# Optimization experiments

Measured on AMD Instinct MI355X. Metric: run time of the kernel, lower is better.

Reference implementation:

```python
import jax, jax.numpy as jnp
import numpy as np

H = 64      # LSTM hidden units
OUT = 10    # dense softmax classes


def setup_inputs() -> dict:
    key = jax.random.key(0)
    k0, k1, k2, k3 = jax.random.split(key, 4)
    B, T, D = 256, 1024, 128
    x = jax.random.normal(k0, (B, T, D), dtype=jnp.float32)
    # small weight scale keeps relu cell state stable over 1024 steps
    W = jax.random.normal(k1, (D, 4 * H), dtype=jnp.float32) * 0.05
    U = jax.random.normal(k2, (H, 4 * H), dtype=jnp.float32) * 0.05
    b = jnp.zeros((4 * H,), jnp.float32)
    Wd = jax.random.normal(k3, (H, OUT), dtype=jnp.float32) * 0.05
    bd = jnp.zeros((OUT,), jnp.float32)
    return {"x": x, "W": W, "U": U, "b": b, "Wd": Wd, "bd": bd}


def hard_sigmoid(z):
    # legacy Keras recurrent_activation default
    return jnp.clip(0.2 * z + 0.5, 0.0, 1.0)


def lstm_last_hidden(x, W, U, b):
    # x: [B,T,D] -> last hidden state [B,H]
    B = x.shape[0]
    xw = jnp.einsum('btd,dg->btg', x, W) + b  # [B,T,4H] input projection, computed once

    def step(carry, xt):
        h, c = carry
        z = xt + h @ U  # [B,4H]
        i = hard_sigmoid(z[:, :H])
        f = hard_sigmoid(z[:, H:2 * H])
        g = jax.nn.relu(z[:, 2 * H:3 * H])   # activation='relu' (candidate)
        o = hard_sigmoid(z[:, 3 * H:])
        c = f * c + i * g
        h = o * jax.nn.relu(c)               # activation='relu' on cell output
        return (h, c), None

    h0 = jnp.zeros((B, H), x.dtype)
    (h, _), _ = jax.lax.scan(step, (h0, h0), jnp.swapaxes(xw, 0, 1))
    return h


def reference(x, W, U, b, Wd, bd):
    h = lstm_last_hidden(x, W, U, b)          # [B,H]
    return jax.nn.softmax(h @ Wd + bd, axis=-1)  # [B,OUT]
```

## Files before the change

### kernel.cpp

```cpp
#include <hip/hip_runtime.h>
#include <hip/hip_bf16.h>

#define Hh   64
#define G4   256
#define Dd   128
#define Bsz  256
#define Tt   1024
#define NOUT 10

typedef __bf16  bf16x8 __attribute__((ext_vector_type(8)));
typedef float   f32x4v __attribute__((ext_vector_type(4)));

__global__ __launch_bounds__(128)
void k0_wt(const float* __restrict__ W, __bf16* __restrict__ Wt) {
    const int n = blockIdx.x;
    const int k = threadIdx.x;
    Wt[(size_t)n * Dd + k] = (__bf16)W[(size_t)k * G4 + n];
}

#define K1_RT 8

__global__ __launch_bounds__(256)
void k1_mfma(const float* __restrict__ x, const __bf16* __restrict__ Wt,
             const float* __restrict__ bias, __bf16* __restrict__ xw) {
    const int tid = threadIdx.x;
    const int w   = tid >> 6;
    const int l   = tid & 63;
    const int r16 = l & 15;
    const int kq  = l >> 4;
    const size_t rowbase = (size_t)blockIdx.x * (16 * K1_RT);

    bf16x8 bfr[4][4];
    float  bval[4];
#pragma unroll
    for (int ct = 0; ct < 4; ++ct) {
        const int col = w * 64 + ct * 16 + r16;
        const __bf16* wp = Wt + (size_t)col * Dd + kq * 8;
#pragma unroll
        for (int kk = 0; kk < 4; ++kk)
            bfr[ct][kk] = *(const bf16x8*)(wp + kk * 32);
        bval[ct] = bias[col];
    }

    for (int rt = 0; rt < K1_RT; ++rt) {
        const size_t arow = rowbase + rt * 16 + r16;
        const float* xr = x + arow * Dd + kq * 8;
        bf16x8 afr[4];
#pragma unroll
        for (int kk = 0; kk < 4; ++kk) {
            const float4 lo = *(const float4*)(xr + kk * 32);
            const float4 hi = *(const float4*)(xr + kk * 32 + 4);
            afr[kk][0] = (__bf16)lo.x; afr[kk][1] = (__bf16)lo.y;
            afr[kk][2] = (__bf16)lo.z; afr[kk][3] = (__bf16)lo.w;
            afr[kk][4] = (__bf16)hi.x; afr[kk][5] = (__bf16)hi.y;
            afr[kk][6] = (__bf16)hi.z; afr[kk][7] = (__bf16)hi.w;
        }
        f32x4v acc[4];
#pragma unroll
        for (int ct = 0; ct < 4; ++ct)
            acc[ct] = (f32x4v){bval[ct], bval[ct], bval[ct], bval[ct]};
#pragma unroll
        for (int ct = 0; ct < 4; ++ct)
#pragma unroll
            for (int kk = 0; kk < 4; ++kk)
                acc[ct] = __builtin_amdgcn_mfma_f32_16x16x32_bf16(
                              afr[kk], bfr[ct][kk], acc[ct], 0, 0, 0);

        const size_t orow0 = rowbase + rt * 16 + kq * 4;
#pragma unroll
        for (int ct = 0; ct < 4; ++ct) {
            const int col = w * 64 + ct * 16 + r16;
#pragma unroll
            for (int r = 0; r < 4; ++r)
                xw[(orow0 + r) * G4 + col] = (__bf16)acc[ct][r];
        }
    }
}

__global__ __launch_bounds__(256)
void k2_scan(const __bf16* __restrict__ xw, const float* __restrict__ U,
             float* __restrict__ hout) {
    const int g = threadIdx.x;
    const int brow = blockIdx.x;

    __shared__ __align__(16) float hs[Hh];
    __shared__ float zs[G4];

    float u[Hh];
#pragma unroll
    for (int j = 0; j < Hh; ++j) u[j] = U[(size_t)j * G4 + g];

    float c = 0.f;
    if (g < Hh) hs[g] = 0.f;

    const __bf16* __restrict__ xwcol = xw + (size_t)brow * Tt * G4 + g;
    float zin = (float)xwcol[0];
    __syncthreads();

    for (int t = 0; t < Tt; ++t) {
        const int tn = (t + 1 < Tt) ? (t + 1) : (Tt - 1);
        const float znext = (float)xwcol[(size_t)tn * G4];
        float a0 = zin, a1 = 0.f, a2 = 0.f, a3 = 0.f;
#pragma unroll
        for (int j = 0; j < Hh; j += 4) {
            const f32x4v h4 = *(const f32x4v*)&hs[j];
            a0 = fmaf(h4[0], u[j + 0], a0);
            a1 = fmaf(h4[1], u[j + 1], a1);
            a2 = fmaf(h4[2], u[j + 2], a2);
            a3 = fmaf(h4[3], u[j + 3], a3);
        }
        zs[g] = (a0 + a1) + (a2 + a3);
        __syncthreads();
        if (g < Hh) {
            const float zi = zs[g], zf = zs[Hh + g], zg = zs[2 * Hh + g], zo = zs[3 * Hh + g];
            const float gi = fminf(fmaxf(0.2f * zi + 0.5f, 0.f), 1.f);
            const float gf = fminf(fmaxf(0.2f * zf + 0.5f, 0.f), 1.f);
            const float gg = fmaxf(zg, 0.f);
            const float go = fminf(fmaxf(0.2f * zo + 0.5f, 0.f), 1.f);
            c = gf * c + gi * gg;
            hs[g] = go * fmaxf(c, 0.f);
        }
        zin = znext;
        __syncthreads();
    }
    if (g < Hh) hout[(size_t)brow * Hh + g] = hs[g];
}

__global__ __launch_bounds__(256)
void k3_dense(const float* __restrict__ hin, const float* __restrict__ Wd,
              const float* __restrict__ bd, float* __restrict__ out) {
    __shared__ float wd[Hh * NOUT];
    __shared__ float bds[NOUT];
    for (int i = threadIdx.x; i < Hh * NOUT; i += blockDim.x) wd[i] = Wd[i];
    if (threadIdx.x < NOUT) bds[threadIdx.x] = bd[threadIdx.x];
    __syncthreads();

    const int r = threadIdx.x;
    if (r < Bsz) {
        float hrow[Hh];
#pragma unroll
        for (int j = 0; j < Hh; ++j) hrow[j] = hin[(size_t)r * Hh + j];
        float logits[NOUT];
#pragma unroll
        for (int o = 0; o < NOUT; ++o) {
            float acc = bds[o];
#pragma unroll
            for (int j = 0; j < Hh; ++j) acc = fmaf(hrow[j], wd[j * NOUT + o], acc);
            logits[o] = acc;
        }
        float m = logits[0];
#pragma unroll
        for (int o = 1; o < NOUT; ++o) m = fmaxf(m, logits[o]);
        float s = 0.f;
#pragma unroll
        for (int o = 0; o < NOUT; ++o) { logits[o] = expf(logits[o] - m); s += logits[o]; }
        const float inv = 1.f / s;
#pragma unroll
        for (int o = 0; o < NOUT; ++o) out[(size_t)r * NOUT + o] = logits[o] * inv;
    }
}

extern "C" void kernel_launch(void* const* d_in, const int* in_sizes, int n_in,
                              void* d_out, int out_size, void* d_ws, size_t ws_size,
                              hipStream_t stream) {
    const float* x  = (const float*)d_in[0];
    const float* W  = (const float*)d_in[1];
    const float* U  = (const float*)d_in[2];
    const float* b  = (const float*)d_in[3];
    const float* Wd = (const float*)d_in[4];
    const float* bd = (const float*)d_in[5];
    float* out = (float*)d_out;

    const size_t xw_bytes = (size_t)Bsz * Tt * G4 * sizeof(__bf16);
    __bf16* xw   = (__bf16*)d_ws;
    float*  hbuf = (float*)((char*)d_ws + xw_bytes);
    __bf16* Wt   = (__bf16*)((char*)d_ws + xw_bytes + (size_t)Bsz * Hh * sizeof(float));

    k0_wt<<<G4, Dd, 0, stream>>>(W, Wt);
    k1_mfma<<<(Bsz * Tt) / (16 * K1_RT), 256, 0, stream>>>(x, Wt, b, xw);
    k2_scan<<<Bsz, 256, 0, stream>>>(xw, U, hbuf);
    k3_dense<<<1, 256, 0, stream>>>(hbuf, Wd, bd, out);
}
```

Before: 572.0 us.

## Permute gate columns so LSTM scan gathers gates via wave shuffles

The projection kernel now writes gate columns in a permuted order, so each wavefront's lanes hold the i, f, g, o pre-activations for the same 16 hidden units. The scan kernel gathers the four gates with cross-lane shuffles and updates the cell state in every lane, instead of going through a shared zs buffer. With a double-buffered h array this removes one of the two block barriers per timestep. All lanes now compute the redundant cell update and a few extra shuffles run per step, traded against less barrier and LDS traffic in the serial 1024-step loop.

```diff
diff --git a/kernel.cpp b/kernel.cpp
--- a/kernel.cpp
+++ b/kernel.cpp
@@ -10,6 +10,7 @@
 
 typedef __bf16  bf16x8 __attribute__((ext_vector_type(8)));
 typedef float   f32x4v __attribute__((ext_vector_type(4)));
+
 
 __global__ __launch_bounds__(128)
 void k0_wt(const float* __restrict__ W, __bf16* __restrict__ Wt) {
@@ -69,10 +70,10 @@
         const size_t orow0 = rowbase + rt * 16 + kq * 4;
 #pragma unroll
         for (int ct = 0; ct < 4; ++ct) {
-            const int col = w * 64 + ct * 16 + r16;
+            const int pcol = ct * 64 + w * 16 + r16;
 #pragma unroll
             for (int r = 0; r < 4; ++r)
-                xw[(orow0 + r) * G4 + col] = (__bf16)acc[ct][r];
+                xw[(orow0 + r) * G4 + pcol] = (__bf16)acc[ct][r];
         }
     }
 }
@@ -80,50 +81,64 @@
 __global__ __launch_bounds__(256)
 void k2_scan(const __bf16* __restrict__ xw, const float* __restrict__ U,
              float* __restrict__ hout) {
-    const int g = threadIdx.x;
+    const int tid = threadIdx.x;
+    const int w   = tid >> 6;
+    const int l   = tid & 63;
+    const int q   = l >> 4;
+    const int m   = l & 15;
     const int brow = blockIdx.x;
 
-    __shared__ __align__(16) float hs[Hh];
-    __shared__ float zs[G4];
+    __shared__ __align__(16) float hs[2][Hh];
 
+    const int ucol = 64 * q + 16 * w + m;
     float u[Hh];
 #pragma unroll
-    for (int j = 0; j < Hh; ++j) u[j] = U[(size_t)j * G4 + g];
+    for (int j = 0; j < Hh; ++j) u[j] = U[(size_t)j * G4 + ucol];
 
     float c = 0.f;
-    if (g < Hh) hs[g] = 0.f;
+    if (tid < Hh) { hs[0][tid] = 0.f; }
 
-    const __bf16* __restrict__ xwcol = xw + (size_t)brow * Tt * G4 + g;
-    float zin = (float)xwcol[0];
+    const __bf16* __restrict__ xwrow = xw + (size_t)brow * Tt * G4 + tid;
+    float zin = (float)xwrow[0];
     __syncthreads();
 
     for (int t = 0; t < Tt; ++t) {
+        const int p  = t & 1;
         const int tn = (t + 1 < Tt) ? (t + 1) : (Tt - 1);
-        const float znext = (float)xwcol[(size_t)tn * G4];
+        const float znext = (float)xwrow[(size_t)tn * G4];
+
         float a0 = zin, a1 = 0.f, a2 = 0.f, a3 = 0.f;
 #pragma unroll
         for (int j = 0; j < Hh; j += 4) {
-            const f32x4v h4 = *(const f32x4v*)&hs[j];
+            const f32x4v h4 = *(const f32x4v*)&hs[p][j];
             a0 = fmaf(h4[0], u[j + 0], a0);
             a1 = fmaf(h4[1], u[j + 1], a1);
             a2 = fmaf(h4[2], u[j + 2], a2);
             a3 = fmaf(h4[3], u[j + 3], a3);
         }
-        zs[g] = (a0 + a1) + (a2 + a3);
-        __syncthreads();
-        if (g < Hh) {
-            const float zi = zs[g], zf = zs[Hh + g], zg = zs[2 * Hh + g], zo = zs[3 * Hh + g];
-            const float gi = fminf(fmaxf(0.2f * zi + 0.5f, 0.f), 1.f);
-            const float gf = fminf(fmaxf(0.2f * zf + 0.5f, 0.f), 1.f);
-            const float gg = fmaxf(zg, 0.f);
-            const float go = fminf(fmaxf(0.2f * zo + 0.5f, 0.f), 1.f);
-            c = gf * c + gi * gg;
-            hs[g] = go * fmaxf(c, 0.f);
-        }
+        const float z = (a0 + a1) + (a2 + a3);
+
+        const float v0 = z;
+        const float v1 = __shfl_xor(z, 16);
+        const float v2 = __shfl_xor(z, 32);
+        const float v3 = __shfl_xor(v1, 32);
+        const float zi = (q == 0) ? v0 : (q == 1) ? v1 : (q == 2) ? v2 : v3;
+        const float zf = (q == 1) ? v0 : (q == 0) ? v1 : (q == 3) ? v2 : v3;
+        const float zg = (q == 2) ? v0 : (q == 3) ? v1 : (q == 0) ? v2 : v3;
+        const float zo = (q == 3) ? v0 : (q == 2) ? v1 : (q == 1) ? v2 : v3;
+
+        const float gi = fminf(fmaxf(0.2f * zi + 0.5f, 0.f), 1.f);
+        const float gf = fminf(fmaxf(0.2f * zf + 0.5f, 0.f), 1.f);
+        const float gg = fmaxf(zg, 0.f);
+        const float go = fminf(fmaxf(0.2f * zo + 0.5f, 0.f), 1.f);
+        c = gf * c + gi * gg;
+        const float h = go * fmaxf(c, 0.f);
+
+        if (q == 0) hs[1 - p][16 * w + m] = h;
         zin = znext;
         __syncthreads();
     }
-    if (g < Hh) hout[(size_t)brow * Hh + g] = hs[g];
+    if (tid < Hh) hout[(size_t)brow * Hh + tid] = hs[0][tid];
 }
 
 __global__ __launch_bounds__(256)
@@ -148,12 +163,12 @@
             for (int j = 0; j < Hh; ++j) acc = fmaf(hrow[j], wd[j * NOUT + o], acc);
             logits[o] = acc;
         }
-        float m = logits[0];
+        float mx = logits[0];
 #pragma unroll
-        for (int o = 1; o < NOUT; ++o) m = fmaxf(m, logits[o]);
+        for (int o = 1; o < NOUT; ++o) mx = fmaxf(mx, logits[o]);
         float s = 0.f;
 #pragma unroll
-        for (int o = 0; o < NOUT; ++o) { logits[o] = expf(logits[o] - m); s += logits[o]; }
+        for (int o = 0; o < NOUT; ++o) { logits[o] = expf(logits[o] - mx); s += logits[o]; }
         const float inv = 1.f / s;
 #pragma unroll
         for (int o = 0; o < NOUT; ++o) out[(size_t)r * NOUT + o] = logits[o] * inv;
```

Result: slower. 619.0 us (+8.2%).

## Cut scan to one barrier per step using redundant gate math and double buffers

Applied to the files above, without the earlier changes.

The recurrent scan kernel now double-buffers the gate pre-activations and the hidden state, so each timestep needs one block barrier instead of two. Every wave computes the gate nonlinearities and cell update for all 64 units and keeps its own private copy of h, which removes the cross-wave dependency on h. Each block now handles two batch rows with 512 threads, and the xw prefetch looks two steps ahead. The cost is redundant elementwise work in every wave and only 128 blocks, which may leave half the CUs idle on a latency-bound loop.

```diff
diff --git a/kernel.cpp b/kernel.cpp
--- a/kernel.cpp
+++ b/kernel.cpp
@@ -71,59 +71,72 @@
         for (int ct = 0; ct < 4; ++ct) {
             const int col = w * 64 + ct * 16 + r16;
 #pragma unroll
-            for (int r = 0; r < 4; ++r)
-                xw[(orow0 + r) * G4 + col] = (__bf16)acc[ct][r];
+            for (int rr = 0; rr < 4; ++rr)
+                xw[(orow0 + rr) * G4 + col] = (__bf16)acc[ct][rr];
         }
     }
 }
 
-__global__ __launch_bounds__(256)
+#define RPB 2
+
+__global__ __launch_bounds__(512)
 void k2_scan(const __bf16* __restrict__ xw, const float* __restrict__ U,
              float* __restrict__ hout) {
-    const int g = threadIdx.x;
-    const int brow = blockIdx.x;
+    const int tid = threadIdx.x;
+    const int r   = tid >> 8;
+    const int g   = tid & 255;
+    const int w4  = g >> 6;
+    const int l   = g & 63;
+    const int brow = blockIdx.x * RPB + r;
 
-    __shared__ __align__(16) float hs[Hh];
-    __shared__ float zs[G4];
+    __shared__ float zs[2][RPB][G4];
+    __shared__ __align__(16) float hs[2][RPB][4][Hh];
 
     float u[Hh];
 #pragma unroll
     for (int j = 0; j < Hh; ++j) u[j] = U[(size_t)j * G4 + g];
 
     float c = 0.f;
-    if (g < Hh) hs[g] = 0.f;
+    hs[0][r][w4][l] = 0.f;
 
-    const __bf16* __restrict__ xwcol = xw + (size_t)brow * Tt * G4 + g;
-    float zin = (float)xwcol[0];
+    const __bf16* __restrict__ xwp = xw + (size_t)brow * Tt * G4 + g;
+    float zcur = (float)xwp[0];
+    float znx  = (float)xwp[G4];
     __syncthreads();
 
     for (int t = 0; t < Tt; ++t) {
-        const int tn = (t + 1 < Tt) ? (t + 1) : (Tt - 1);
-        const float znext = (float)xwcol[(size_t)tn * G4];
-        float a0 = zin, a1 = 0.f, a2 = 0.f, a3 = 0.f;
+        const int p  = t & 1;
+        const int t2 = (t + 2 < Tt) ? (t + 2) : (Tt - 1);
+        const float zpp = (float)xwp[(size_t)t2 * G4];
+
+        const float* __restrict__ hp = hs[p][r][w4];
+        float a0 = zcur, a1 = 0.f, a2 = 0.f, a3 = 0.f;
 #pragma unroll
         for (int j = 0; j < Hh; j += 4) {
-            const f32x4v h4 = *(const f32x4v*)&hs[j];
+            const f32x4v h4 = *(const f32x4v*)&hp[j];
             a0 = fmaf(h4[0], u[j + 0], a0);
             a1 = fmaf(h4[1], u[j + 1], a1);
             a2 = fmaf(h4[2], u[j + 2], a2);
             a3 = fmaf(h4[3], u[j + 3], a3);
         }
-        zs[g] = (a0 + a1) + (a2 + a3);
+        zs[p][r][g] = (a0 + a1) + (a2 + a3);
         __syncthreads();
-        if (g < Hh) {
-            const float zi = zs[g], zf = zs[Hh + g], zg = zs[2 * Hh + g], zo = zs[3 * Hh + g];
-            const float gi = fminf(fmaxf(0.2f * zi + 0.5f, 0.f), 1.f);
-            const float gf = fminf(fmaxf(0.2f * zf + 0.5f, 0.f), 1.f);
-            const float gg = fmaxf(zg, 0.f);
-            const float go = fminf(fmaxf(0.2f * zo + 0.5f, 0.f), 1.f);
-            c = gf * c + gi * gg;
-            hs[g] = go * fmaxf(c, 0.f);
-        }
-        zin = znext;
-        __syncthreads();
+
+        const float zi = zs[p][r][l];
+        const float zf = zs[p][r][64 + l];
+        const float zg = zs[p][r][128 + l];
+        const float zo = zs[p][r][192 + l];
+        const float gi = fminf(fmaxf(0.2f * zi + 0.5f, 0.f), 1.f);
+        const float gf = fminf(fmaxf(0.2f * zf + 0.5f, 0.f), 1.f);
+        const float gg = fmaxf(zg, 0.f);
+        const float go = fminf(fmaxf(0.2f * zo + 0.5f, 0.f), 1.f);
+        c = gf * c + gi * gg;
+        const float h = go * fmaxf(c, 0.f);
+
+        hs[1 - p][r][w4][l] = h;
+        zcur = znx; znx = zpp;
     }
-    if (g < Hh) hout[(size_t)brow * Hh + g] = hs[g];
+    if (w4 == 0) hout[(size_t)brow * Hh + l] = hs[0][r][0][l];
 }
 
 __global__ __launch_bounds__(256)
@@ -148,12 +161,12 @@
             for (int j = 0; j < Hh; ++j) acc = fmaf(hrow[j], wd[j * NOUT + o], acc);
             logits[o] = acc;
         }
-        float m = logits[0];
+        float mx = logits[0];
 #pragma unroll
-        for (int o = 1; o < NOUT; ++o) m = fmaxf(m, logits[o]);
+        for (int o = 1; o < NOUT; ++o) mx = fmaxf(mx, logits[o]);
         float s = 0.f;
 #pragma unroll
-        for (int o = 0; o < NOUT; ++o) { logits[o] = expf(logits[o] - m); s += logits[o]; }
+        for (int o = 0; o < NOUT; ++o) { logits[o] = expf(logits[o] - mx); s += logits[o]; }
         const float inv = 1.f / s;
 #pragma unroll
         for (int o = 0; o < NOUT; ++o) out[(size_t)r * NOUT + o] = logits[o] * inv;
@@ -178,6 +191,6 @@
 
     k0_wt<<<G4, Dd, 0, stream>>>(W, Wt);
     k1_mfma<<<(Bsz * Tt) / (16 * K1_RT), 256, 0, stream>>>(x, Wt, b, xw);
-    k2_scan<<<Bsz, 256, 0, stream>>>(xw, U, hbuf);
+    k2_scan<<<Bsz / RPB, 512, 0, stream>>>(xw, U, hbuf);
     k3_dense<<<1, 256, 0, stream>>>(hbuf, Wd, bd, out);
 }
```

New measurement: 672.7 us. 1.18x slower.

## Run LSTM recurrence with MFMA over 16-row batches and permuted gate columns

Applied to the files above, without the earlier changes.

The scan kernel now processes 16 batch rows per single-wave block and computes h@U with bf16 MFMA instructions instead of per-thread scalar FMAs through shared memory. Gate columns are permuted and the hard-sigmoid scale and offset are folded into W, U and bias, so MFMA outputs land directly in the lanes that apply the gate math, with no LDS round trip or barriers. The xw input is prefetched two timesteps ahead in registers. The trade-offs are bf16 rounding of U and h inside the recurrence, and only 16 blocks for 256 batch rows, which leaves most of the GPU idle.

```diff
diff --git a/kernel.cpp b/kernel.cpp
--- a/kernel.cpp
+++ b/kernel.cpp
@@ -11,11 +11,25 @@
 typedef __bf16  bf16x8 __attribute__((ext_vector_type(8)));
 typedef float   f32x4v __attribute__((ext_vector_type(4)));
 
+__device__ __forceinline__ int rho_origcol(int rho) {
+    const int g  = rho >> 6;
+    const int s  = (rho >> 5) & 1;
+    const int d2 = (rho >> 4) & 1;
+    const int kq = (rho >> 2) & 3;
+    const int dl = rho & 3;
+    return g * 64 + (32 * s + 8 * kq + 4 * d2 + dl);
+}
+
 __global__ __launch_bounds__(128)
-void k0_wt(const float* __restrict__ W, __bf16* __restrict__ Wt) {
-    const int n = blockIdx.x;
-    const int k = threadIdx.x;
-    Wt[(size_t)n * Dd + k] = (__bf16)W[(size_t)k * G4 + n];
+void k0_prep(const float* __restrict__ W, const float* __restrict__ b,
+             __bf16* __restrict__ Wt, float* __restrict__ bias2) {
+    const int rho = blockIdx.x;
+    const int k   = threadIdx.x;
+    const int col = rho_origcol(rho);
+    const bool isg = ((rho >> 6) == 2);
+    const float sc = isg ? 1.f : 0.2f;
+    Wt[(size_t)rho * Dd + k] = (__bf16)(sc * W[(size_t)k * G4 + col]);
+    if (k == 0) bias2[rho] = sc * b[col] + (isg ? 0.f : 0.5f);
 }
 
 #define K1_RT 8
@@ -71,59 +85,111 @@
         for (int ct = 0; ct < 4; ++ct) {
             const int col = w * 64 + ct * 16 + r16;
 #pragma unroll
-            for (int r = 0; r < 4; ++r)
-                xw[(orow0 + r) * G4 + col] = (__bf16)acc[ct][r];
-        }
-    }
-}
-
-__global__ __launch_bounds__(256)
+            for (int rr = 0; rr < 4; ++rr)
+                xw[(orow0 + rr) * G4 + col] = (__bf16)acc[ct][rr];
+        }
+    }
+}
+
+__global__ __launch_bounds__(64)
 void k2_scan(const __bf16* __restrict__ xw, const float* __restrict__ U,
              float* __restrict__ hout) {
-    const int g = threadIdx.x;
-    const int brow = blockIdx.x;
-
-    __shared__ __align__(16) float hs[Hh];
-    __shared__ float zs[G4];
-
-    float u[Hh];
-#pragma unroll
-    for (int j = 0; j < Hh; ++j) u[j] = U[(size_t)j * G4 + g];
-
-    float c = 0.f;
-    if (g < Hh) hs[g] = 0.f;
-
-    const __bf16* __restrict__ xwcol = xw + (size_t)brow * Tt * G4 + g;
-    float zin = (float)xwcol[0];
-    __syncthreads();
-
-    for (int t = 0; t < Tt; ++t) {
-        const int tn = (t + 1 < Tt) ? (t + 1) : (Tt - 1);
-        const float znext = (float)xwcol[(size_t)tn * G4];
-        float a0 = zin, a1 = 0.f, a2 = 0.f, a3 = 0.f;
-#pragma unroll
-        for (int j = 0; j < Hh; j += 4) {
-            const f32x4v h4 = *(const f32x4v*)&hs[j];
-            a0 = fmaf(h4[0], u[j + 0], a0);
-            a1 = fmaf(h4[1], u[j + 1], a1);
-            a2 = fmaf(h4[2], u[j + 2], a2);
-            a3 = fmaf(h4[3], u[j + 3], a3);
-        }
-        zs[g] = (a0 + a1) + (a2 + a3);
-        __syncthreads();
-        if (g < Hh) {
-            const float zi = zs[g], zf = zs[Hh + g], zg = zs[2 * Hh + g], zo = zs[3 * Hh + g];
-            const float gi = fminf(fmaxf(0.2f * zi + 0.5f, 0.f), 1.f);
-            const float gf = fminf(fmaxf(0.2f * zf + 0.5f, 0.f), 1.f);
-            const float gg = fmaxf(zg, 0.f);
-            const float go = fminf(fmaxf(0.2f * zo + 0.5f, 0.f), 1.f);
-            c = gf * c + gi * gg;
-            hs[g] = go * fmaxf(c, 0.f);
-        }
-        zin = znext;
-        __syncthreads();
-    }
-    if (g < Hh) hout[(size_t)brow * Hh + g] = hs[g];
+    const int l  = threadIdx.x & 63;
+    const int kq = l >> 4;
+    const int m  = l & 15;
+    const int b0 = blockIdx.x * 16;
+
+    bf16x8 au[16][2];
+#pragma unroll
+    for (int tt = 0; tt < 16; ++tt) {
+        const int rho = 16 * tt + m;
+        const int col = rho_origcol(rho);
+        const float sc = ((rho >> 6) == 2) ? 1.f : 0.2f;
+#pragma unroll
+        for (int ks = 0; ks < 2; ++ks)
+#pragma unroll
+            for (int j = 0; j < 8; ++j)
+                au[tt][ks][j] = (__bf16)(sc * U[(size_t)(ks * 32 + kq * 8 + j) * G4 + col]);
+    }
+
+    float c[2][2][4];
+    float h[2][2][4];
+#pragma unroll
+    for (int s = 0; s < 2; ++s)
+#pragma unroll
+        for (int d2 = 0; d2 < 2; ++d2)
+#pragma unroll
+            for (int dl = 0; dl < 4; ++dl) { c[s][d2][dl] = 0.f; h[s][d2][dl] = 0.f; }
+
+    bf16x8 bh0 = {};
+    bf16x8 bh1 = {};
+
+    const char* pbase = (const char*)xw + ((size_t)(b0 + m) * Tt) * (G4 * 2) + kq * 8;
+
+    uint2 pf[2][16];
+#pragma unroll
+    for (int s = 0; s < 2; ++s)
+#pragma unroll
+        for (int tt = 0; tt < 16; ++tt)
+            pf[s][tt] = *(const uint2*)(pbase + s * 512 + tt * 32);
+
+    for (int t0 = 0; t0 < Tt; t0 += 2) {
+        const char* pc = pbase + (size_t)t0 * 512;
+#pragma unroll
+        for (int s = 0; s < 2; ++s) {
+            f32x4v acc[16];
+#pragma unroll
+            for (int tt = 0; tt < 16; ++tt) {
+                const uint2 d = pf[s][tt];
+                acc[tt][0] = __builtin_bit_cast(float, d.x << 16);
+                acc[tt][1] = __builtin_bit_cast(float, d.x & 0xFFFF0000u);
+                acc[tt][2] = __builtin_bit_cast(float, d.y << 16);
+                acc[tt][3] = __builtin_bit_cast(float, d.y & 0xFFFF0000u);
+            }
+#pragma unroll
+            for (int tt = 0; tt < 16; ++tt)
+                pf[s][tt] = *(const uint2*)(pc + (s + 2) * 512 + tt * 32);
+
+#pragma unroll
+            for (int tt = 0; tt < 16; ++tt) {
+                acc[tt] = __builtin_amdgcn_mfma_f32_16x16x32_bf16(au[tt][0], bh0, acc[tt], 0, 0, 0);
+                acc[tt] = __builtin_amdgcn_mfma_f32_16x16x32_bf16(au[tt][1], bh1, acc[tt], 0, 0, 0);
+            }
+
+#pragma unroll
+            for (int s2 = 0; s2 < 2; ++s2)
+#pragma unroll
+                for (int d2 = 0; d2 < 2; ++d2) {
+                    const int ti = 2 * s2 + d2;
+#pragma unroll
+                    for (int dl = 0; dl < 4; ++dl) {
+                        const float gi = fminf(fmaxf(acc[ti][dl],      0.f), 1.f);
+                        const float gf = fminf(fmaxf(acc[4 + ti][dl],  0.f), 1.f);
+                        const float gg = fmaxf(acc[8 + ti][dl], 0.f);
+                        const float go = fminf(fmaxf(acc[12 + ti][dl], 0.f), 1.f);
+                        const float cc = fmaf(gf, c[s2][d2][dl], gi * gg);
+                        c[s2][d2][dl] = cc;
+                        h[s2][d2][dl] = go * fmaxf(cc, 0.f);
+                    }
+                }
+
+#pragma unroll
+            for (int d2 = 0; d2 < 2; ++d2)
+#pragma unroll
+                for (int dl = 0; dl < 4; ++dl) {
+                    bh0[4 * d2 + dl] = (__bf16)h[0][d2][dl];
+                    bh1[4 * d2 + dl] = (__bf16)h[1][d2][dl];
+                }
+        }
+    }
+
+#pragma unroll
+    for (int s2 = 0; s2 < 2; ++s2)
+#pragma unroll
+        for (int d2 = 0; d2 < 2; ++d2)
+#pragma unroll
+            for (int dl = 0; dl < 4; ++dl)
+                hout[(size_t)(b0 + m) * Hh + 32 * s2 + 8 * kq + 4 * d2 + dl] = h[s2][d2][dl];
 }
 
 __global__ __launch_bounds__(256)
@@ -148,12 +214,12 @@
             for (int j = 0; j < Hh; ++j) acc = fmaf(hrow[j], wd[j * NOUT + o], acc);
             logits[o] = acc;
         }
-        float m = logits[0];
-#pragma unroll
-        for (int o = 1; o < NOUT; ++o) m = fmaxf(m, logits[o]);
+        float mx = logits[0];
+#pragma unroll
+        for (int o = 1; o < NOUT; ++o) mx = fmaxf(mx, logits[o]);
         float s = 0.f;
 #pragma unroll
-        for (int o = 0; o < NOUT; ++o) { logits[o] = expf(logits[o] - m); s += logits[o]; }
+        for (int o = 0; o < NOUT; ++o) { logits[o] = expf(logits[o] - mx); s += logits[o]; }
         const float inv = 1.f / s;
 #pragma unroll
         for (int o = 0; o < NOUT; ++o) out[(size_t)r * NOUT + o] = logits[o] * inv;
@@ -172,12 +238,13 @@
     float* out = (float*)d_out;
 
     const size_t xw_bytes = (size_t)Bsz * Tt * G4 * sizeof(__bf16);
-    __bf16* xw   = (__bf16*)d_ws;
-    float*  hbuf = (float*)((char*)d_ws + xw_bytes);
-    __bf16* Wt   = (__bf16*)((char*)d_ws + xw_bytes + (size_t)Bsz * Hh * sizeof(float));
-
-    k0_wt<<<G4, Dd, 0, stream>>>(W, Wt);
-    k1_mfma<<<(Bsz * Tt) / (16 * K1_RT), 256, 0, stream>>>(x, Wt, b, xw);
-    k2_scan<<<Bsz, 256, 0, stream>>>(xw, U, hbuf);
+    __bf16* xw    = (__bf16*)d_ws;
+    float*  hbuf  = (float*)((char*)d_ws + xw_bytes);
+    __bf16* Wt    = (__bf16*)((char*)hbuf + (size_t)Bsz * Hh * sizeof(float));
+    float*  bias2 = (float*)((char*)Wt + (size_t)G4 * Dd * sizeof(__bf16));
+
+    k0_prep<<<G4, Dd, 0, stream>>>(W, b, Wt, bias2);
+    k1_mfma<<<(Bsz * Tt) / (16 * K1_RT), 256, 0, stream>>>(x, Wt, bias2, xw);
+    k2_scan<<<Bsz / 16, 64, 0, stream>>>(xw, U, hbuf);
     k3_dense<<<1, 256, 0, stream>>>(hbuf, Wd, bd, out);
 }
```

Measured after the change: 2.196 ms. 3.84x slower.
